# Kernel tuning notes

Measured on AMD Instinct MI355X. Metric: run time of the kernel, lower is better.

Reference implementation:

```python
import jax, jax.numpy as jnp
import numpy as np

NEG = -1e10
EPS = 1e-5
H = 4  # num_heads


def layer_norm(y, g, b):
    m = jnp.mean(y, axis=-1, keepdims=True)
    v = jnp.mean((y - m) ** 2, axis=-1, keepdims=True)
    return (y - m) * jax.lax.rsqrt(v + EPS) * g + b


def setup_inputs() -> dict:
    key = jax.random.key(0)
    B, N, C = 16, 1024, 256
    ks = jax.random.split(key, 12)
    std = 0.1  # matches trunc_normal_(std=0.1) init
    inp = {
        "x": jax.random.normal(ks[0], (B, N, C), jnp.float32),
        "K": jax.random.normal(ks[1], (B, N, N), jnp.float32),
        "n1": jax.random.randint(ks[2], (B,), 8, 33),
        "n2": jax.random.randint(ks[3], (B,), 8, 33),
        "qkv_w": jax.random.normal(ks[4], (3 * C, C), jnp.float32) * std,
        "qkv_b": jnp.zeros((3 * C,), jnp.float32),
        "proj_w": jax.random.normal(ks[5], (C, C), jnp.float32) * std,
        "proj_b": jnp.zeros((C,), jnp.float32),
        "ln1_g": jnp.ones((C,), jnp.float32),
        "ln1_b": jnp.zeros((C,), jnp.float32),
        "ln2_g": jnp.ones((C,), jnp.float32),
        "ln2_b": jnp.zeros((C,), jnp.float32),
        "fc1_w": jax.random.normal(ks[6], (4 * C, C), jnp.float32) * std,
        "fc1_b": jnp.zeros((4 * C,), jnp.float32),
        "fc2_w": jax.random.normal(ks[7], (C, 4 * C), jnp.float32) * std,
        "fc2_b": jnp.zeros((C,), jnp.float32),
    }
    return inp


def reference(x, K, n1, n2, qkv_w, qkv_b, proj_w, proj_b,
              ln1_g, ln1_b, ln2_g, ln2_b, fc1_w, fc1_b, fc2_w, fc2_b):
    B, N, C = x.shape
    D = C // H
    scale = D ** -0.5

    # --- attention block ---
    h = layer_norm(x, ln1_g, ln1_b)
    qkv = (h @ qkv_w.T + qkv_b).reshape(B, N, 3, H, D)
    qkv = jnp.transpose(qkv, (2, 0, 3, 1, 4))  # [3,B,H,N,D]
    q, k, v = qkv[0], qkv[1], qkv[2]

    attn = jnp.einsum('bhnd,bhmd->bhnm', q, k) * scale  # [B,H,N,N]

    # per-sample dynamic block mask: rows>=n1*n2 fully masked; cols>=n1*n2 masked
    nrc = (n1 * n2)[:, None]                  # [B,1]
    invalid = jnp.arange(N)[None, :] >= nrc   # [B,N]
    mask = invalid[:, :, None] | invalid[:, None, :]  # [B,N,N]
    attn = jnp.where(mask[:, None], NEG, attn)
    attn = attn + K[:, None]                  # broadcast K over heads

    a = jax.nn.softmax(attn, axis=-1)
    o = jnp.einsum('bhnm,bhmd->bhnd', a, v)
    o = jnp.transpose(o, (0, 2, 1, 3)).reshape(B, N, C)
    x = x + (o @ proj_w.T + proj_b)

    # --- MLP block (exact GELU as torch nn.GELU) ---
    h2 = layer_norm(x, ln2_g, ln2_b)
    m = jax.nn.gelu(h2 @ fc1_w.T + fc1_b, approximate=False)
    m = m @ fc2_w.T + fc2_b
    return x + m
```

## Files before the change

kernel.cpp:

```cpp
#include <hip/hip_runtime.h>
#include <math.h>
#include <stdint.h>

constexpr int Bc = 16, Nn = 1024, Cc = 256, Hh = 4;
constexpr int Mrows = Bc * Nn;
constexpr float EPSV = 1e-5f;

typedef __attribute__((ext_vector_type(4))) float f32x4;
typedef __attribute__((ext_vector_type(8))) short bf16x8;

__device__ inline float wave_reduce_sum(float v) {
#pragma unroll
  for (int m = 32; m >= 1; m >>= 1) v += __shfl_xor(v, m);
  return v;
}

__device__ inline short f2bf(float f) {
  uint32_t u = __builtin_bit_cast(uint32_t, f);
  u = (u + 0x7fffu + ((u >> 16) & 1u)) >> 16;
  return (short)u;
}
__device__ inline float bf2f(short s) {
  uint32_t u = ((uint32_t)(uint16_t)s) << 16;
  return __builtin_bit_cast(float, u);
}

__device__ inline float fexp(float x) {
  return __builtin_amdgcn_exp2f(x * 1.4426950408889634f);
}

__device__ inline float gelu_fast(float x) {
  float x2 = x * x;
  float u = x * (0.7978845608028654f + 0.0356774081f * x2);
  float e = __builtin_amdgcn_exp2f(u * 2.8853900817779268f);
  return x * (1.f - __builtin_amdgcn_rcpf(e + 1.f));
}

#define GLDS(gptr, lptr)                                             \
  __builtin_amdgcn_global_load_lds(                                  \
      (const __attribute__((address_space(1))) void*)(gptr),         \
      (__attribute__((address_space(3))) void*)(lptr), 16, 0, 0)

__global__ __launch_bounds__(256)
void cvt_bf16(const float* __restrict__ src, short* __restrict__ dst, int n) {
  int i = (blockIdx.x * 256 + threadIdx.x) * 4;
  if (i >= n) return;
  float4 v = *(const float4*)(src + i);
  short4 o;
  o.x = f2bf(v.x); o.y = f2bf(v.y); o.z = f2bf(v.z); o.w = f2bf(v.w);
  *(short4*)(dst + i) = o;
}

__global__ __launch_bounds__(256)
void ln_kernel(const float* __restrict__ x, const float* __restrict__ g,
               const float* __restrict__ b, short* __restrict__ h) {
  int row = blockIdx.x * 4 + (threadIdx.x >> 6);
  int lane = threadIdx.x & 63;
  const float4* xr = (const float4*)(x + (size_t)row * Cc);
  float4 v = xr[lane];
  float s = v.x + v.y + v.z + v.w;
  float sq = v.x * v.x + v.y * v.y + v.z * v.z + v.w * v.w;
  s = wave_reduce_sum(s);
  sq = wave_reduce_sum(sq);
  float mean = s * (1.f / Cc);
  float var = sq * (1.f / Cc) - mean * mean;
  float inv = rsqrtf(var + EPSV);
  float4 gg = ((const float4*)g)[lane];
  float4 bb = ((const float4*)b)[lane];
  short4 o;
  o.x = f2bf((v.x - mean) * inv * gg.x + bb.x);
  o.y = f2bf((v.y - mean) * inv * gg.y + bb.y);
  o.z = f2bf((v.z - mean) * inv * gg.z + bb.z);
  o.w = f2bf((v.w - mean) * inv * gg.w + bb.w);
  *(short4*)(h + (size_t)row * Cc + lane * 4) = o;
}

__global__ __launch_bounds__(256)
void qkv_mfma(const short* __restrict__ A, const short* __restrict__ Bw,
              const float* __restrict__ bias, short* __restrict__ qkp,
              short* __restrict__ vtp) {
  __shared__ __align__(16) short As[128 * 64];
  __shared__ __align__(16) short Bs[128 * 64];
  int t = threadIdx.x;
  int w = t >> 6, lane = t & 63;
  int wm = w >> 1, wn = w & 1;
  int l16 = lane & 15, lhi = lane >> 4;
  int m0 = blockIdx.y * 128, n0 = blockIdx.x * 128;
  const bool vblk = (n0 >= 512);
  f32x4 acc[4][4] = {};

  for (int k0 = 0; k0 < 256; k0 += 64) {
    __syncthreads();
#pragma unroll
    for (int i = 0; i < 4; ++i) {
      int cc = i * 256 + t;
      int r = cc >> 3, sl = cc & 7, ssl = sl ^ (r & 7);
      GLDS(A + (size_t)(m0 + r) * 256 + k0 + ssl * 8, &As[cc * 8]);
      GLDS(Bw + (size_t)(n0 + r) * 256 + k0 + ssl * 8, &Bs[cc * 8]);
    }
    asm volatile("s_waitcnt vmcnt(0)" ::: "memory");
    __syncthreads();
    if (!vblk) {
#pragma unroll
      for (int ks = 0; ks < 2; ++ks) {
        bf16x8 af[4], bg[4];
#pragma unroll
        for (int mi = 0; mi < 4; ++mi) {
          int row = wm * 64 + mi * 16 + l16;
          af[mi] = *(const bf16x8*)&As[row * 64 + ((ks * 32 + lhi * 8) ^ ((row & 7) << 3))];
        }
#pragma unroll
        for (int ni = 0; ni < 4; ++ni) {
          int row = wn * 64 + ni * 16 + l16;
          bg[ni] = *(const bf16x8*)&Bs[row * 64 + ((ks * 32 + lhi * 8) ^ ((row & 7) << 3))];
        }
#pragma unroll
        for (int mi = 0; mi < 4; ++mi)
#pragma unroll
          for (int ni = 0; ni < 4; ++ni)
            acc[mi][ni] = __builtin_amdgcn_mfma_f32_16x16x32_bf16(
                af[mi], bg[ni], acc[mi][ni], 0, 0, 0);
      }
    } else {
#pragma unroll
      for (int ks = 0; ks < 2; ++ks) {
        bf16x8 af[4], bg[4];
#pragma unroll
        for (int mi = 0; mi < 4; ++mi) {
          int row = wm * 64 + mi * 16 + l16;
          af[mi] = *(const bf16x8*)&As[row * 64 + ((ks * 32 + lhi * 8) ^ ((row & 7) << 3))];
        }
#pragma unroll
        for (int ni = 0; ni < 4; ++ni) {
          int row = wn * 64 + ni * 16 + l16;
          bg[ni] = *(const bf16x8*)&Bs[row * 64 + ((ks * 32 + lhi * 8) ^ ((row & 7) << 3))];
        }
#pragma unroll
        for (int mi = 0; mi < 4; ++mi)
#pragma unroll
          for (int ni = 0; ni < 4; ++ni)
            acc[mi][ni] = __builtin_amdgcn_mfma_f32_16x16x32_bf16(
                bg[ni], af[mi], acc[mi][ni], 0, 0, 0);
      }
    }
  }

  if (!vblk) {
    const bool isq = (n0 < 256);
#pragma unroll
    for (int mi = 0; mi < 4; ++mi) {
      int mbase = m0 + wm * 64 + mi * 16 + lhi * 4;
#pragma unroll
      for (int ni = 0; ni < 4; ++ni) {
        int n = n0 + wn * 64 + ni * 16 + l16;
        int s = n >> 8, hh = (n >> 6) & 3, d = n & 63;
        float bv = bias[n];
#pragma unroll
        for (int r = 0; r < 4; ++r) {
          int m = mbase + r;
          int b = m >> 10, rw = m & 1023;
          float v = acc[mi][ni][r] + bv;
          if (isq) v *= 0.125f;
          qkp[(size_t)s * 4194304 + (((size_t)(b * 4 + hh)) * 1024 + rw) * 64 + d] = f2bf(v);
        }
      }
    }
  } else {
#pragma unroll
    for (int mi = 0; mi < 4; ++mi) {
#pragma unroll
      for (int ni = 0; ni < 4; ++ni) {
#pragma unroll
        for (int r = 0; r < 4; ++r) {
          int n = n0 + wn * 64 + ni * 16 + lhi * 4 + r;
          int hh = (n >> 6) & 3, d = n & 63;
          int m = m0 + wm * 64 + mi * 16 + l16;
          int b = m >> 10, rw = m & 1023;
          float v = acc[mi][ni][r] + bias[n];
          vtp[(((size_t)(b * 4 + hh)) * 64 + d) * 1024 + rw] = f2bf(v);
        }
      }
    }
  }
}

__global__ __launch_bounds__(256)
void vmean_kernel(const short* __restrict__ vt, short* __restrict__ vmb) {
  __shared__ float part[64][4];
  int bh = blockIdx.x;
  int d = threadIdx.x >> 2, seg = threadIdx.x & 3;
  const short* p = vt + (size_t)bh * 65536 + (size_t)d * 1024 + seg * 256;
  float s = 0.f;
  for (int i = 0; i < 256; i += 8) {
    bf16x8 v = *(const bf16x8*)(p + i);
#pragma unroll
    for (int j = 0; j < 8; ++j) s += bf2f(v[j]);
  }
  part[d][seg] = s;
  __syncthreads();
  if (threadIdx.x < 64) {
    int dd = threadIdx.x;
    float tot = part[dd][0] + part[dd][1] + part[dd][2] + part[dd][3];
    vmb[bh * 64 + dd] = f2bf(tot * (1.f / 1024.f));
  }
}

__global__ __launch_bounds__(256)
void fattn_mfma(const short* __restrict__ qpk, const short* __restrict__ kpk,
                const short* __restrict__ vt, const float* __restrict__ Kmat,
                const int* __restrict__ n1, const int* __restrict__ n2,
                const short* __restrict__ vmb, short* __restrict__ o) {
  int bh = blockIdx.y, b = bh >> 2, hh = bh & 3;
  int row0 = blockIdx.x * 64;
  int nc = n1[b] * n2[b];
  int t = threadIdx.x;
  __shared__ short vms[64];
  if (t < 64) vms[t] = vmb[bh * 64 + t];
  __syncthreads();
  if (row0 >= nc) {
    for (int idx = t; idx < 4096; idx += 256) {
      int r = idx >> 6, d = idx & 63;
      o[((size_t)(b * 1024 + row0 + r)) * 256 + hh * 64 + d] = vms[d];
    }
    return;
  }
  __shared__ __align__(16) short Ks[2][64 * 64];
  __shared__ __align__(16) short Vs[2][64 * 64];
  __shared__ __align__(16) short Ps[64 * 64];
  int w = t >> 6, lane = t & 63, l16 = lane & 15, lhi = lane >> 4;

  constexpr float LOG2E = 1.4426950408889634f;
  constexpr float MREF = 12.0f;

  const short* qb = qpk + (size_t)bh * 65536 + (size_t)(row0 + w * 16 + l16) * 64;
  bf16x8 qf0 = *(const bf16x8*)(qb + lhi * 8);
  bf16x8 qf1 = *(const bf16x8*)(qb + 32 + lhi * 8);

  f32x4 accO[4] = {};
  float lsum[4] = {};
  const float* Kb = Kmat + (size_t)b * 1048576 + (size_t)(row0 + w * 16) * 1024;

  float kvp[16];

#pragma unroll
  for (int i = 0; i < 2; ++i) {
    int cc = i * 256 + t;
    int r = cc >> 3, sl = cc & 7, ssl = sl ^ (r & 7);
    GLDS(kpk + (size_t)bh * 65536 + (size_t)(0 + r) * 64 + ssl * 8, &Ks[0][cc * 8]);
    GLDS(vt + (size_t)bh * 65536 + (size_t)r * 1024 + 0 + ssl * 8, &Vs[0][cc * 8]);
  }
#pragma unroll
  for (int ni = 0; ni < 4; ++ni)
#pragma unroll
    for (int r = 0; r < 4; ++r)
      kvp[ni * 4 + r] =
          (Kb[(size_t)(lhi * 4 + r) * 1024 + 0 + ni * 16 + l16] - MREF) * LOG2E;

  int cur = 0;
  for (int j0 = 0; j0 < nc; j0 += 64, cur ^= 1) {
    asm volatile("s_waitcnt vmcnt(0)" ::: "memory");
    __syncthreads();

    float kvc[16];
#pragma unroll
    for (int i = 0; i < 16; ++i) kvc[i] = kvp[i];
    int jn = j0 + 64;
    if (jn < nc) {
      int nxt = cur ^ 1;
#pragma unroll
      for (int i = 0; i < 2; ++i) {
        int cc = i * 256 + t;
        int r = cc >> 3, sl = cc & 7, ssl = sl ^ (r & 7);
        GLDS(kpk + (size_t)bh * 65536 + (size_t)(jn + r) * 64 + ssl * 8, &Ks[nxt][cc * 8]);
        GLDS(vt + (size_t)bh * 65536 + (size_t)r * 1024 + jn + ssl * 8, &Vs[nxt][cc * 8]);
      }
#pragma unroll
      for (int ni = 0; ni < 4; ++ni)
#pragma unroll
        for (int r = 0; r < 4; ++r)
          kvp[ni * 4 + r] =
              (Kb[(size_t)(lhi * 4 + r) * 1024 + jn + ni * 16 + l16] - MREF) * LOG2E;
    }

    f32x4 accS[4] = {};
#pragma unroll
    for (int ks = 0; ks < 2; ++ks) {
#pragma unroll
      for (int ni = 0; ni < 4; ++ni) {
        int row = ni * 16 + l16;
        bf16x8 kf = *(const bf16x8*)&Ks[cur][row * 64 + (((ks * 4 + lhi) ^ (row & 7)) << 3)];
        accS[ni] = __builtin_amdgcn_mfma_f32_16x16x32_bf16(
            ks ? qf1 : qf0, kf, accS[ni], 0, 0, 0);
      }
    }

#pragma unroll
    for (int ni = 0; ni < 4; ++ni) {
      bool valid = (j0 + ni * 16 + l16) < nc;
#pragma unroll
      for (int r = 0; r < 4; ++r) {
        float e = __builtin_amdgcn_exp2f(fmaf(accS[ni][r], LOG2E, kvc[ni * 4 + r]));
        e = valid ? e : 0.f;
        lsum[r] += e;
        int prow = w * 16 + lhi * 4 + r;
        int col = ni * 16 + l16;
        Ps[prow * 64 + ((((col >> 3) ^ (prow & 7)) << 3) | (col & 7))] = f2bf(e);
      }
    }

#pragma unroll
    for (int ks = 0; ks < 2; ++ks) {
      int prow = w * 16 + l16;
      bf16x8 pf = *(const bf16x8*)&Ps[prow * 64 + (((ks * 4 + lhi) ^ (prow & 7)) << 3)];
#pragma unroll
      for (int ni = 0; ni < 4; ++ni) {
        int vrow = ni * 16 + l16;
        bf16x8 vf = *(const bf16x8*)&Vs[cur][vrow * 64 + (((ks * 4 + lhi) ^ (vrow & 7)) << 3)];
        accO[ni] = __builtin_amdgcn_mfma_f32_16x16x32_bf16(pf, vf, accO[ni], 0, 0, 0);
      }
    }
  }

#pragma unroll
  for (int r = 0; r < 4; ++r) {
    lsum[r] += __shfl_xor(lsum[r], 1);
    lsum[r] += __shfl_xor(lsum[r], 2);
    lsum[r] += __shfl_xor(lsum[r], 4);
    lsum[r] += __shfl_xor(lsum[r], 8);
  }

#pragma unroll
  for (int ni = 0; ni < 4; ++ni) {
#pragma unroll
    for (int r = 0; r < 4; ++r) {
      int row = row0 + w * 16 + lhi * 4 + r;
      int d = ni * 16 + l16;
      short ov;
      if (row < nc) ov = f2bf(accO[ni][r] * (1.f / lsum[r]));
      else ov = vms[d];
      o[((size_t)(b * 1024 + row)) * 256 + hh * 64 + d] = ov;
    }
  }
}

template <bool GELU, bool RES, bool OUTF, bool OUTB>
__global__ __launch_bounds__(256)
void gemm_mfma(const short* __restrict__ A, const short* __restrict__ Bw,
               const float* __restrict__ bias, const float* __restrict__ resid,
               float* __restrict__ Cf, short* __restrict__ Cb,
               int M, int Nd, int Kd) {
  __shared__ __align__(16) short As[128 * 64];
  __shared__ __align__(16) short Bs[128 * 64];
  int t = threadIdx.x;
  int w = t >> 6, lane = t & 63;
  int wm = w >> 1, wn = w & 1;
  int l16 = lane & 15, lhi = lane >> 4;
  int m0 = blockIdx.y * 128, n0 = blockIdx.x * 128;
  f32x4 acc[4][4] = {};

  for (int k0 = 0; k0 < Kd; k0 += 64) {
    __syncthreads();
#pragma unroll
    for (int i = 0; i < 4; ++i) {
      int cc = i * 256 + t;
      int r = cc >> 3, sl = cc & 7, ssl = sl ^ (r & 7);
      GLDS(A + (size_t)(m0 + r) * Kd + k0 + ssl * 8, &As[cc * 8]);
      GLDS(Bw + (size_t)(n0 + r) * Kd + k0 + ssl * 8, &Bs[cc * 8]);
    }
    asm volatile("s_waitcnt vmcnt(0)" ::: "memory");
    __syncthreads();
#pragma unroll
    for (int ks = 0; ks < 2; ++ks) {
      bf16x8 af[4], bg[4];
#pragma unroll
      for (int mi = 0; mi < 4; ++mi) {
        int row = wm * 64 + mi * 16 + l16;
        af[mi] = *(const bf16x8*)&As[row * 64 + ((ks * 32 + lhi * 8) ^ ((row & 7) << 3))];
      }
#pragma unroll
      for (int ni = 0; ni < 4; ++ni) {
        int row = wn * 64 + ni * 16 + l16;
        bg[ni] = *(const bf16x8*)&Bs[row * 64 + ((ks * 32 + lhi * 8) ^ ((row & 7) << 3))];
      }
#pragma unroll
      for (int mi = 0; mi < 4; ++mi)
#pragma unroll
        for (int ni = 0; ni < 4; ++ni)
          acc[mi][ni] = __builtin_amdgcn_mfma_f32_16x16x32_bf16(
              af[mi], bg[ni], acc[mi][ni], 0, 0, 0);
    }
  }
#pragma unroll
  for (int mi = 0; mi < 4; ++mi) {
    int rbase = m0 + wm * 64 + mi * 16 + lhi * 4;
#pragma unroll
    for (int ni = 0; ni < 4; ++ni) {
      int n = n0 + wn * 64 + ni * 16 + l16;
      float bv = bias[n];
#pragma unroll
      for (int r = 0; r < 4; ++r) {
        int m = rbase + r;
        float v = acc[mi][ni][r] + bv;
        if (GELU) v = gelu_fast(v);
        size_t idx = (size_t)m * Nd + n;
        if (RES) v += resid[idx];
        if (OUTF) Cf[idx] = v;
        if (OUTB) Cb[idx] = f2bf(v);
      }
    }
  }
}

extern "C" void kernel_launch(void* const* d_in, const int* in_sizes, int n_in,
                              void* d_out, int out_size, void* d_ws, size_t ws_size,
                              hipStream_t stream) {
  const float* x      = (const float*)d_in[0];
  const float* Kmat   = (const float*)d_in[1];
  const int*   n1     = (const int*)d_in[2];
  const int*   n2     = (const int*)d_in[3];
  const float* qkv_w  = (const float*)d_in[4];
  const float* qkv_b  = (const float*)d_in[5];
  const float* proj_w = (const float*)d_in[6];
  const float* proj_b = (const float*)d_in[7];
  const float* ln1_g  = (const float*)d_in[8];
  const float* ln1_b  = (const float*)d_in[9];
  const float* ln2_g  = (const float*)d_in[10];
  const float* ln2_b  = (const float*)d_in[11];
  const float* fc1_w  = (const float*)d_in[12];
  const float* fc1_b  = (const float*)d_in[13];
  const float* fc2_w  = (const float*)d_in[14];
  const float* fc2_b  = (const float*)d_in[15];
  float* out = (float*)d_out;

  char* ws = (char*)d_ws;
  constexpr size_t MB = 1024 * 1024;
  short* hb    = (short*)ws;
  short* qkp   = (short*)(ws + 8 * MB);
  short* vtp   = (short*)(ws + 24 * MB);
  short* m1    = (short*)(ws + 8 * MB);
  short* vmb   = (short*)(ws + 40 * MB);
  short* wqkv  = (short*)(ws + 41 * MB);
  short* wproj = (short*)(ws + 42 * MB);
  short* wfc1  = (short*)(ws + 43 * MB);
  short* wfc2  = (short*)(ws + 44 * MB);
  short* obuf  = hb;
  short* qpk   = qkp;
  short* kpk   = qkp + 4194304;

  cvt_bf16<<<dim3(768 * 256 / 1024), 256, 0, stream>>>(qkv_w, wqkv, 768 * 256);
  cvt_bf16<<<dim3(256 * 256 / 1024), 256, 0, stream>>>(proj_w, wproj, 256 * 256);
  cvt_bf16<<<dim3(1024 * 256 / 1024), 256, 0, stream>>>(fc1_w, wfc1, 1024 * 256);
  cvt_bf16<<<dim3(256 * 1024 / 1024), 256, 0, stream>>>(fc2_w, wfc2, 256 * 1024);
  ln_kernel<<<dim3(Mrows / 4), 256, 0, stream>>>(x, ln1_g, ln1_b, hb);
  qkv_mfma<<<dim3(6, 128), 256, 0, stream>>>(hb, wqkv, qkv_b, qkp, vtp);
  vmean_kernel<<<dim3(Bc * Hh), 256, 0, stream>>>(vtp, vmb);
  fattn_mfma<<<dim3(Nn / 64, Bc * Hh), 256, 0, stream>>>(
      qpk, kpk, vtp, Kmat, n1, n2, vmb, obuf);
  gemm_mfma<false, true, true, false><<<dim3(2, 128), 256, 0, stream>>>(
      obuf, wproj, proj_b, x, out, nullptr, Mrows, 256, 256);
  ln_kernel<<<dim3(Mrows / 4), 256, 0, stream>>>(out, ln2_g, ln2_b, hb);
  gemm_mfma<true, false, false, true><<<dim3(8, 128), 256, 0, stream>>>(
      hb, wfc1, fc1_b, nullptr, nullptr, m1, Mrows, 1024, 256);
  gemm_mfma<false, true, true, false><<<dim3(2, 128), 256, 0, stream>>>(
      m1, wfc2, fc2_b, out, out, nullptr, Mrows, 256, 1024);
}
```

Before: 150.4 us.

## Pre-pack K bias into MFMA fragment layout, fuse weight casts, smaller-tile output GEMMs

Adds a kpack kernel that rewrites the needed valid region of the K bias matrix into a per-16-row-tile, MFMA-fragment-ordered, pre-scaled layout. The attention kernel can then load each lane's bias values as contiguous float4 vectors instead of scattered strided scalars. The packed path only runs when the workspace is at least 112 MB, otherwise the old path is used. The four weight-conversion launches are merged into one kernel, and the N=256 output GEMMs (proj and fc2) move to a 64-row tile kernel with twice as many blocks for better occupancy. The cost is an extra pass over K, extra workspace, and a non-pipelined 64-row GEMM.

```diff
diff --git a/kernel.cpp b/kernel.cpp
--- a/kernel.cpp
+++ b/kernel.cpp
@@ -23,10 +23,6 @@
 __device__ inline float bf2f(short s) {
   uint32_t u = ((uint32_t)(uint16_t)s) << 16;
   return __builtin_bit_cast(float, u);
-}
-
-__device__ inline float fexp(float x) {
-  return __builtin_amdgcn_exp2f(x * 1.4426950408889634f);
 }
 
 __device__ inline float gelu_fast(float x) {
@@ -42,13 +38,23 @@
       (__attribute__((address_space(3))) void*)(lptr), 16, 0, 0)
 
 __global__ __launch_bounds__(256)
-void cvt_bf16(const float* __restrict__ src, short* __restrict__ dst, int n) {
-  int i = (blockIdx.x * 256 + threadIdx.x) * 4;
-  if (i >= n) return;
-  float4 v = *(const float4*)(src + i);
+void cvt_all(const float* __restrict__ s0, short* __restrict__ d0,
+             const float* __restrict__ s1, short* __restrict__ d1,
+             const float* __restrict__ s2, short* __restrict__ d2,
+             const float* __restrict__ s3, short* __restrict__ d3) {
+  int bid = blockIdx.x;
+  const float* s;
+  short* d;
+  int base;
+  if (bid < 192)      { s = s0; d = d0; base = bid; }
+  else if (bid < 256) { s = s1; d = d1; base = bid - 192; }
+  else if (bid < 512) { s = s2; d = d2; base = bid - 256; }
+  else                { s = s3; d = d3; base = bid - 512; }
+  int i = (base * 256 + threadIdx.x) * 4;
+  float4 v = *(const float4*)(s + i);
   short4 o;
   o.x = f2bf(v.x); o.y = f2bf(v.y); o.z = f2bf(v.z); o.w = f2bf(v.w);
-  *(short4*)(dst + i) = o;
+  *(short4*)(d + i) = o;
 }
 
 __global__ __launch_bounds__(256)
@@ -206,8 +212,39 @@
 }
 
 __global__ __launch_bounds__(256)
+void kpack(const float* __restrict__ Kmat, const int* __restrict__ n1,
+           const int* __restrict__ n2, float* __restrict__ pkb) {
+  int b = blockIdx.x >> 4, jt = blockIdx.x & 15;
+  int nc = n1[b] * n2[b];
+  if (jt * 64 >= nc) return;
+  int nrt = (nc + 15) >> 4;
+  __shared__ float tile[16][65];
+  int t = threadIdx.x;
+  const float* src = Kmat + (size_t)b * 1048576 + jt * 64;
+  float* dst = pkb + (size_t)b * 1048576 + (size_t)jt * 65536;
+  int ni = t >> 6, lane = t & 63, lhi = lane >> 4, l16 = lane & 15;
+  for (int rt = 0; rt < nrt; ++rt) {
+    __syncthreads();
+#pragma unroll
+    for (int p = 0; p < 4; ++p) {
+      int rr = p * 4 + (t >> 6);
+      int c = t & 63;
+      tile[rr][c] = src[(size_t)(rt * 16 + rr) * 1024 + c];
+    }
+    __syncthreads();
+    f32x4 ov;
+#pragma unroll
+    for (int r = 0; r < 4; ++r)
+      ov[r] = (tile[lhi * 4 + r][ni * 16 + l16] - 12.0f) * 1.4426950408889634f;
+    *(f32x4*)(dst + (size_t)rt * 1024 + t * 4) = ov;
+  }
+}
+
+template <bool PACKED>
+__global__ __launch_bounds__(256)
 void fattn_mfma(const short* __restrict__ qpk, const short* __restrict__ kpk,
                 const short* __restrict__ vt, const float* __restrict__ Kmat,
+                const float* __restrict__ pkb,
                 const int* __restrict__ n1, const int* __restrict__ n2,
                 const short* __restrict__ vmb, short* __restrict__ o) {
   int bh = blockIdx.y, b = bh >> 2, hh = bh & 3;
@@ -238,32 +275,39 @@
 
   f32x4 accO[4] = {};
   float lsum[4] = {};
+  int rt16 = blockIdx.x * 4 + w;
   const float* Kb = Kmat + (size_t)b * 1048576 + (size_t)(row0 + w * 16) * 1024;
-
-  float kvp[16];
+  const float* Pb = pkb + (size_t)b * 1048576 + (size_t)rt16 * 1024 + lane * 4;
+
+  f32x4 kvp[4];
 
 #pragma unroll
   for (int i = 0; i < 2; ++i) {
     int cc = i * 256 + t;
     int r = cc >> 3, sl = cc & 7, ssl = sl ^ (r & 7);
-    GLDS(kpk + (size_t)bh * 65536 + (size_t)(0 + r) * 64 + ssl * 8, &Ks[0][cc * 8]);
-    GLDS(vt + (size_t)bh * 65536 + (size_t)r * 1024 + 0 + ssl * 8, &Vs[0][cc * 8]);
-  }
-#pragma unroll
-  for (int ni = 0; ni < 4; ++ni)
-#pragma unroll
-    for (int r = 0; r < 4; ++r)
-      kvp[ni * 4 + r] =
-          (Kb[(size_t)(lhi * 4 + r) * 1024 + 0 + ni * 16 + l16] - MREF) * LOG2E;
+    GLDS(kpk + (size_t)bh * 65536 + (size_t)r * 64 + ssl * 8, &Ks[0][cc * 8]);
+    GLDS(vt + (size_t)bh * 65536 + (size_t)r * 1024 + ssl * 8, &Vs[0][cc * 8]);
+  }
+  if (PACKED) {
+#pragma unroll
+    for (int ni = 0; ni < 4; ++ni) kvp[ni] = *(const f32x4*)(Pb + ni * 256);
+  } else {
+#pragma unroll
+    for (int ni = 0; ni < 4; ++ni)
+#pragma unroll
+      for (int r = 0; r < 4; ++r)
+        kvp[ni][r] =
+            (Kb[(size_t)(lhi * 4 + r) * 1024 + ni * 16 + l16] - MREF) * LOG2E;
+  }
 
   int cur = 0;
   for (int j0 = 0; j0 < nc; j0 += 64, cur ^= 1) {
     asm volatile("s_waitcnt vmcnt(0)" ::: "memory");
     __syncthreads();
 
-    float kvc[16];
-#pragma unroll
-    for (int i = 0; i < 16; ++i) kvc[i] = kvp[i];
+    f32x4 kvc[4];
+#pragma unroll
+    for (int i = 0; i < 4; ++i) kvc[i] = kvp[i];
     int jn = j0 + 64;
     if (jn < nc) {
       int nxt = cur ^ 1;
@@ -274,12 +318,18 @@
         GLDS(kpk + (size_t)bh * 65536 + (size_t)(jn + r) * 64 + ssl * 8, &Ks[nxt][cc * 8]);
         GLDS(vt + (size_t)bh * 65536 + (size_t)r * 1024 + jn + ssl * 8, &Vs[nxt][cc * 8]);
       }
-#pragma unroll
-      for (int ni = 0; ni < 4; ++ni)
-#pragma unroll
-        for (int r = 0; r < 4; ++r)
-          kvp[ni * 4 + r] =
-              (Kb[(size_t)(lhi * 4 + r) * 1024 + jn + ni * 16 + l16] - MREF) * LOG2E;
+      if (PACKED) {
+#pragma unroll
+        for (int ni = 0; ni < 4; ++ni)
+          kvp[ni] = *(const f32x4*)(Pb + (size_t)(jn >> 6) * 65536 + ni * 256);
+      } else {
+#pragma unroll
+        for (int ni = 0; ni < 4; ++ni)
+#pragma unroll
+          for (int r = 0; r < 4; ++r)
+            kvp[ni][r] =
+                (Kb[(size_t)(lhi * 4 + r) * 1024 + jn + ni * 16 + l16] - MREF) * LOG2E;
+      }
     }
 
     f32x4 accS[4] = {};
@@ -299,7 +349,7 @@
       bool valid = (j0 + ni * 16 + l16) < nc;
 #pragma unroll
       for (int r = 0; r < 4; ++r) {
-        float e = __builtin_amdgcn_exp2f(fmaf(accS[ni][r], LOG2E, kvc[ni * 4 + r]));
+        float e = __builtin_amdgcn_exp2f(fmaf(accS[ni][r], LOG2E, kvc[ni][r]));
         e = valid ? e : 0.f;
         lsum[r] += e;
         int prow = w * 16 + lhi * 4 + r;
@@ -396,6 +446,78 @@
 #pragma unroll
     for (int ni = 0; ni < 4; ++ni) {
       int n = n0 + wn * 64 + ni * 16 + l16;
+      float bv = bias[n];
+#pragma unroll
+      for (int r = 0; r < 4; ++r) {
+        int m = rbase + r;
+        float v = acc[mi][ni][r] + bv;
+        if (GELU) v = gelu_fast(v);
+        size_t idx = (size_t)m * Nd + n;
+        if (RES) v += resid[idx];
+        if (OUTF) Cf[idx] = v;
+        if (OUTB) Cb[idx] = f2bf(v);
+      }
+    }
+  }
+}
+
+template <bool GELU, bool RES, bool OUTF, bool OUTB>
+__global__ __launch_bounds__(256)
+void gemm64_mfma(const short* __restrict__ A, const short* __restrict__ Bw,
+                 const float* __restrict__ bias, const float* __restrict__ resid,
+                 float* __restrict__ Cf, short* __restrict__ Cb,
+                 int M, int Nd, int Kd) {
+  __shared__ __align__(16) short As[64 * 64];
+  __shared__ __align__(16) short Bs[128 * 64];
+  int t = threadIdx.x;
+  int w = t >> 6, lane = t & 63;
+  int l16 = lane & 15, lhi = lane >> 4;
+  int m0 = blockIdx.y * 64, n0 = blockIdx.x * 128;
+  f32x4 acc[4][2] = {};
+
+  for (int k0 = 0; k0 < Kd; k0 += 64) {
+    __syncthreads();
+#pragma unroll
+    for (int i = 0; i < 2; ++i) {
+      int cc = i * 256 + t;
+      int r = cc >> 3, sl = cc & 7, ssl = sl ^ (r & 7);
+      GLDS(A + (size_t)(m0 + r) * Kd + k0 + ssl * 8, &As[cc * 8]);
+    }
+#pragma unroll
+    for (int i = 0; i < 4; ++i) {
+      int cc = i * 256 + t;
+      int r = cc >> 3, sl = cc & 7, ssl = sl ^ (r & 7);
+      GLDS(Bw + (size_t)(n0 + r) * Kd + k0 + ssl * 8, &Bs[cc * 8]);
+    }
+    asm volatile("s_waitcnt vmcnt(0)" ::: "memory");
+    __syncthreads();
+#pragma unroll
+    for (int ks = 0; ks < 2; ++ks) {
+      bf16x8 af[4], bg[2];
+#pragma unroll
+      for (int mi = 0; mi < 4; ++mi) {
+        int row = mi * 16 + l16;
+        af[mi] = *(const bf16x8*)&As[row * 64 + ((ks * 32 + lhi * 8) ^ ((row & 7) << 3))];
+      }
+#pragma unroll
+      for (int ni = 0; ni < 2; ++ni) {
+        int row = w * 32 + ni * 16 + l16;
+        bg[ni] = *(const bf16x8*)&Bs[row * 64 + ((ks * 32 + lhi * 8) ^ ((row & 7) << 3))];
+      }
+#pragma unroll
+      for (int mi = 0; mi < 4; ++mi)
+#pragma unroll
+        for (int ni = 0; ni < 2; ++ni)
+          acc[mi][ni] = __builtin_amdgcn_mfma_f32_16x16x32_bf16(
+              af[mi], bg[ni], acc[mi][ni], 0, 0, 0);
+    }
+  }
+#pragma unroll
+  for (int mi = 0; mi < 4; ++mi) {
+    int rbase = m0 + mi * 16 + lhi * 4;
+#pragma unroll
+    for (int ni = 0; ni < 2; ++ni) {
+      int n = n0 + w * 32 + ni * 16 + l16;
       float bv = bias[n];
 #pragma unroll
       for (int r = 0; r < 4; ++r) {
@@ -443,24 +565,31 @@
   short* wproj = (short*)(ws + 42 * MB);
   short* wfc1  = (short*)(ws + 43 * MB);
   short* wfc2  = (short*)(ws + 44 * MB);
+  float* pkb   = (float*)(ws + 48 * MB);
   short* obuf  = hb;
   short* qpk   = qkp;
   short* kpk   = qkp + 4194304;
 
-  cvt_bf16<<<dim3(768 * 256 / 1024), 256, 0, stream>>>(qkv_w, wqkv, 768 * 256);
-  cvt_bf16<<<dim3(256 * 256 / 1024), 256, 0, stream>>>(proj_w, wproj, 256 * 256);
-  cvt_bf16<<<dim3(1024 * 256 / 1024), 256, 0, stream>>>(fc1_w, wfc1, 1024 * 256);
-  cvt_bf16<<<dim3(256 * 1024 / 1024), 256, 0, stream>>>(fc2_w, wfc2, 256 * 1024);
+  const bool packed = ws_size >= (size_t)112 * MB;
+
+  cvt_all<<<dim3(768), 256, 0, stream>>>(qkv_w, wqkv, proj_w, wproj,
+                                         fc1_w, wfc1, fc2_w, wfc2);
   ln_kernel<<<dim3(Mrows / 4), 256, 0, stream>>>(x, ln1_g, ln1_b, hb);
+  if (packed)
+    kpack<<<dim3(256), 256, 0, stream>>>(Kmat, n1, n2, pkb);
   qkv_mfma<<<dim3(6, 128), 256, 0, stream>>>(hb, wqkv, qkv_b, qkp, vtp);
   vmean_kernel<<<dim3(Bc * Hh), 256, 0, stream>>>(vtp, vmb);
-  fattn_mfma<<<dim3(Nn / 64, Bc * Hh), 256, 0, stream>>>(
-      qpk, kpk, vtp, Kmat, n1, n2, vmb, obuf);
-  gemm_mfma<false, true, true, false><<<dim3(2, 128), 256, 0, stream>>>(
+  if (packed)
+    fattn_mfma<true><<<dim3(Nn / 64, Bc * Hh), 256, 0, stream>>>(
+        qpk, kpk, vtp, Kmat, pkb, n1, n2, vmb, obuf);
+  else
+    fattn_mfma<false><<<dim3(Nn / 64, Bc * Hh), 256, 0, stream>>>(
+        qpk, kpk, vtp, Kmat, pkb, n1, n2, vmb, obuf);
+  gemm64_mfma<false, true, true, false><<<dim3(2, 256), 256, 0, stream>>>(
       obuf, wproj, proj_b, x, out, nullptr, Mrows, 256, 256);
   ln_kernel<<<dim3(Mrows / 4), 256, 0, stream>>>(out, ln2_g, ln2_b, hb);
   gemm_mfma<true, false, false, true><<<dim3(8, 128), 256, 0, stream>>>(
       hb, wfc1, fc1_b, nullptr, nullptr, m1, Mrows, 1024, 256);
-  gemm_mfma<false, true, true, false><<<dim3(2, 128), 256, 0, stream>>>(
+  gemm64_mfma<false, true, true, false><<<dim3(2, 256), 256, 0, stream>>>(
       m1, wfc2, fc2_b, out, out, nullptr, Mrows, 256, 1024);
 }
```

After: 164.7 us. 1.1x slower.
